# Optimization experiments

Hardware: AMD Instinct MI355X
Metric: run time of the kernel (lower is better)

The kernel has to match this reference:

```python
import jax, jax.numpy as jnp
import numpy as np


def setup_inputs() -> dict:
    key = jax.random.key(0)
    ks = jax.random.split(key, 5)
    bs, ntok, dm, nh = 4, 256, 64, 4
    x = jax.random.normal(ks[0], (bs, ntok, dm), dtype=jnp.float32)
    wk = jax.random.uniform(ks[1], (nh, dm), dtype=jnp.float32)
    wqv_w = jax.random.normal(ks[2], (3 * nh * dm, dm), dtype=jnp.float32) * 0.02
    wqv_b = jnp.zeros((3 * nh * dm,), dtype=jnp.float32)
    fanin_w = jax.random.normal(ks[3], (dm, dm), dtype=jnp.float32) * 0.02
    fanin_b = jnp.zeros((dm,), dtype=jnp.float32)
    return {"x": x, "wk": wk, "wqv_w": wqv_w, "wqv_b": wqv_b,
            "fanin_w": fanin_w, "fanin_b": fanin_b,
            "layer": 0, "use_dp": 0, "doplot": 0}


def reference(x, wk, wqv_w, wqv_b, fanin_w, fanin_b, layer, use_dp, doplot):
    # L1-attention path (use_dp=False, doplot=False) of ResidualAttentionBlock.forward
    bs, ntok, dm = x.shape
    nh = wk.shape[0]
    delta = 0.2
    # wqv projection -> q, vf, vb each [b, t, nh, dm] (d_head == d_model in this module)
    v = (x @ wqv_w.T + wqv_b).reshape(bs, ntok, 3 * nh, dm)
    q, vf, vb = v[:, :, :nh, :], v[:, :, nh:2 * nh, :], v[:, :, 2 * nh:, :]
    k = x[:, :, None, :] * wk[None, None, :, :]   # [b, s, h, w]
    q = q * wk[None, None, :, :]                   # [b, d, h, w]
    # L1Attn: score[b, s, d, h] = -sum_w |q[b,d,h,w] - k[b,s,h,w]| / sqrt(w);
    # module then negates -> positive scaled L1 distance, applies Huber-like remap, negates back.
    dist = jnp.sum(jnp.abs(q[:, None, :, :, :] - k[:, :, None, :, :]), axis=-1)
    dist = dist / jnp.sqrt(jnp.asarray(dm, dtype=x.dtype))  # [b, s, d, h]
    hub = jnp.where(dist < delta, 0.5 * dist * dist, delta * (dist - 0.5 * delta))
    a = -hub
    af = jax.nn.softmax(a, axis=1)                 # softmax over src tokens
    # (ab = softmax over dst and bb are computed in the original but unused: b = bf)
    bf = jnp.einsum('bsdh,bshw->bdhw', af, vf)     # aggregate values over src
    b = jnp.sum(bf, axis=2)                        # sum over heads -> [b, t, dm]
    y = b * jax.nn.sigmoid(1.702 * b)              # QuickGELU
    y = y @ fanin_w.T + fanin_b
    return x + y
```

## Files before the change

### kernel.cpp

```cpp
#include <hip/hip_runtime.h>

#define NT 256
#define DM 64
#define NH 4

__global__ __launch_bounds__(256) void k_proj(const float* __restrict__ x,
                                              const float* __restrict__ wk,
                                              const float* __restrict__ wqv_w,
                                              const float* __restrict__ wqv_b,
                                              float* __restrict__ q_s,
                                              float* __restrict__ vf)
{
    __shared__ float xs[4 * DM];
    const int tid  = threadIdx.x;
    const int tok0 = blockIdx.x * 4;

    if (tid < 64)
        reinterpret_cast<float4*>(xs)[tid] =
            reinterpret_cast<const float4*>(x + tok0 * DM)[tid];
    __syncthreads();

    const float4* wr0 = reinterpret_cast<const float4*>(wqv_w + tid * DM);
    const float4* wr1 = reinterpret_cast<const float4*>(wqv_w + (tid + 256) * DM);
    float a0[4] = {0.f, 0.f, 0.f, 0.f};
    float a1[4] = {0.f, 0.f, 0.f, 0.f};

#pragma unroll
    for (int c4 = 0; c4 < 16; ++c4) {
        const float4 wa = wr0[c4];
        const float4 wb = wr1[c4];
#pragma unroll
        for (int t = 0; t < 4; ++t) {
            const float4 xv = reinterpret_cast<const float4*>(xs + t * DM)[c4];
            a0[t] += xv.x * wa.x + xv.y * wa.y + xv.z * wa.z + xv.w * wa.w;
            a1[t] += xv.x * wb.x + xv.y * wb.y + xv.z * wb.z + xv.w * wb.w;
        }
    }

    const int h = tid >> 6, w = tid & 63;
    const float ba = wqv_b[tid];
    const float bb = wqv_b[tid + 256];
    const float kw = wk[h * DM + w];
#pragma unroll
    for (int t = 0; t < 4; ++t) {
        const int g = tok0 + t, b = g >> 8, tt = g & 255;
        const int o = ((b * NH + h) * NT + tt) * DM + w;
        q_s[o] = (a0[t] + ba) * kw;
        vf[o]  =  a1[t] + bb;
    }
}

#define KS_LD 66
#define AF_LD 258

__global__ __launch_bounds__(256) void k_attn(const float* __restrict__ x,
                                              const float* __restrict__ wk,
                                              const float* __restrict__ q_s,
                                              const float* __restrict__ vf,
                                              float* __restrict__ bf)
{
    __shared__ float ks[64 * KS_LD];
    __shared__ float af[16 * AF_LD];
    __shared__ float vfs[NT * DM];
    __shared__ float part[4 * 16 * DM];

    const int tid = threadIdx.x;
    const int qt  = blockIdx.x;
    const int bh  = blockIdx.y;
    const int b   = bh >> 2, h = bh & 3;
    const int qg  = tid >> 5;
    const int kg  = tid & 31;

    float q0[DM], q1[DM];
    {
        const float4* p0 = reinterpret_cast<const float4*>(
            q_s + ((b * NH + h) * NT + qt * 16 + qg * 2) * DM);
        const float4* p1 = p0 + 16;
#pragma unroll
        for (int i = 0; i < 16; ++i) {
            const float4 u = p0[i];
            q0[4*i] = u.x; q0[4*i+1] = u.y; q0[4*i+2] = u.z; q0[4*i+3] = u.w;
            const float4 v = p1[i];
            q1[4*i] = v.x; q1[4*i+1] = v.y; q1[4*i+2] = v.z; q1[4*i+3] = v.w;
        }
    }

    const float4* wkr = reinterpret_cast<const float4*>(wk + h * DM);

    float dacc[2][8];
#pragma unroll
    for (int j = 0; j < 8; ++j) { dacc[0][j] = 0.f; dacc[1][j] = 0.f; }

    for (int cc = 0; cc < 4; ++cc) {
        __syncthreads();
        {
            const int row = tid >> 2, c0 = (tid & 3) * 16;
            const float4* xp = reinterpret_cast<const float4*>(
                x + ((b * NT) + cc * 64 + row) * DM + c0);
            float* kp = ks + row * KS_LD + c0;
#pragma unroll
            for (int i = 0; i < 4; ++i) {
                const float4 v  = xp[i];
                const float4 wv = wkr[(c0 >> 2) + i];
                reinterpret_cast<float2*>(kp)[2*i]     = make_float2(v.x * wv.x, v.y * wv.y);
                reinterpret_cast<float2*>(kp)[2*i + 1] = make_float2(v.z * wv.z, v.w * wv.w);
            }
        }
        __syncthreads();
#pragma unroll
        for (int k2 = 0; k2 < 2; ++k2) {
            const float2* kp = reinterpret_cast<const float2*>(ks + (kg + 32 * k2) * KS_LD);
            float d0 = 0.f, d1 = 0.f;
#pragma unroll
            for (int c2 = 0; c2 < 32; ++c2) {
                const float2 kv = kp[c2];
                d0 += fabsf(q0[2*c2] - kv.x) + fabsf(q0[2*c2+1] - kv.y);
                d1 += fabsf(q1[2*c2] - kv.x) + fabsf(q1[2*c2+1] - kv.y);
            }
            dacc[0][cc * 2 + k2] = d0;
            dacc[1][cc * 2 + k2] = d1;
        }
    }

    {
        const float4* vp = reinterpret_cast<const float4*>(vf + (b * NH + h) * NT * DM);
#pragma unroll
        for (int it = 0; it < 16; ++it) {
            const int qidx = it * 256 + tid;
            reinterpret_cast<float4*>(vfs)[qidx] = vp[qidx];
        }
    }

    const float delta = 0.2f;
    float aa0[8], aa1[8];
    float m0 = -1e30f, m1 = -1e30f;
#pragma unroll
    for (int j = 0; j < 8; ++j) {
        float d  = dacc[0][j] * 0.125f;
        float hb = (d < delta) ? 0.5f * d * d : delta * (d - 0.5f * delta);
        aa0[j] = -hb; m0 = fmaxf(m0, aa0[j]);
        d  = dacc[1][j] * 0.125f;
        hb = (d < delta) ? 0.5f * d * d : delta * (d - 0.5f * delta);
        aa1[j] = -hb; m1 = fmaxf(m1, aa1[j]);
    }
#pragma unroll
    for (int mask = 1; mask < 32; mask <<= 1) {
        m0 = fmaxf(m0, __shfl_xor(m0, mask, 32));
        m1 = fmaxf(m1, __shfl_xor(m1, mask, 32));
    }
    float s0 = 0.f, s1 = 0.f;
#pragma unroll
    for (int j = 0; j < 8; ++j) {
        aa0[j] = __expf(aa0[j] - m0); s0 += aa0[j];
        aa1[j] = __expf(aa1[j] - m1); s1 += aa1[j];
    }
#pragma unroll
    for (int mask = 1; mask < 32; mask <<= 1) {
        s0 += __shfl_xor(s0, mask, 32);
        s1 += __shfl_xor(s1, mask, 32);
    }
    const float rs0 = 1.f / s0, rs1 = 1.f / s1;
#pragma unroll
    for (int j = 0; j < 8; ++j) {
        const int skey = (j >> 1) * 64 + (j & 1) * 32 + kg;
        af[(qg * 2 + 0) * AF_LD + skey] = aa0[j] * rs0;
        af[(qg * 2 + 1) * AF_LD + skey] = aa1[j] * rs1;
    }
    __syncthreads();

    {
        const int wq  = tid & 15;
        const int qg4 = (tid >> 4) & 3;
        const int sr  = tid >> 6;

        float4 acc0 = {0,0,0,0}, acc1 = {0,0,0,0}, acc2 = {0,0,0,0}, acc3 = {0,0,0,0};
        const float* afb = af + (qg4 * 4) * AF_LD + sr * 64;
        const float* vb  = vfs + (sr * 64) * DM + wq * 4;
#pragma unroll
        for (int s = 0; s < 64; ++s) {
            const float4 v = *reinterpret_cast<const float4*>(vb + s * DM);
            const float a0 = afb[0 * AF_LD + s];
            const float a1 = afb[1 * AF_LD + s];
            const float a2 = afb[2 * AF_LD + s];
            const float a3 = afb[3 * AF_LD + s];
            acc0.x += a0 * v.x; acc0.y += a0 * v.y; acc0.z += a0 * v.z; acc0.w += a0 * v.w;
            acc1.x += a1 * v.x; acc1.y += a1 * v.y; acc1.z += a1 * v.z; acc1.w += a1 * v.w;
            acc2.x += a2 * v.x; acc2.y += a2 * v.y; acc2.z += a2 * v.z; acc2.w += a2 * v.w;
            acc3.x += a3 * v.x; acc3.y += a3 * v.y; acc3.z += a3 * v.z; acc3.w += a3 * v.w;
        }
        float* pp = part + (sr * 16 + qg4 * 4) * DM + wq * 4;
        *reinterpret_cast<float4*>(pp + 0 * DM) = acc0;
        *reinterpret_cast<float4*>(pp + 1 * DM) = acc1;
        *reinterpret_cast<float4*>(pp + 2 * DM) = acc2;
        *reinterpret_cast<float4*>(pp + 3 * DM) = acc3;
    }
    __syncthreads();

    {
        const int q = tid >> 4, w4 = tid & 15;
        const float* pp = part + q * DM + w4 * 4;
        float4 r0 = *reinterpret_cast<const float4*>(pp);
        const float4 r1 = *reinterpret_cast<const float4*>(pp + 16 * DM);
        const float4 r2 = *reinterpret_cast<const float4*>(pp + 32 * DM);
        const float4 r3 = *reinterpret_cast<const float4*>(pp + 48 * DM);
        r0.x += r1.x + r2.x + r3.x;
        r0.y += r1.y + r2.y + r3.y;
        r0.z += r1.z + r2.z + r3.z;
        r0.w += r1.w + r2.w + r3.w;
        float* op = bf + ((b * NH + h) * NT + qt * 16 + q) * DM + w4 * 4;
        *reinterpret_cast<float4*>(op) = r0;
    }
}

__global__ __launch_bounds__(256) void k_out(const float* __restrict__ x,
                                             const float* __restrict__ bf,
                                             const float* __restrict__ fanin_w,
                                             const float* __restrict__ fanin_b,
                                             float* __restrict__ out)
{
    __shared__ float fw[64 * 68];
    __shared__ float ys[4 * DM];

    const int tid  = threadIdx.x;
    const int tok0 = blockIdx.x * 4;

#pragma unroll
    for (int it = 0; it < 4; ++it) {
        const int qidx = it * 256 + tid;
        const int row = qidx >> 4, cq = qidx & 15;
        *reinterpret_cast<float4*>(fw + row * 68 + cq * 4) =
            reinterpret_cast<const float4*>(fanin_w)[qidx];
    }
    {
        const int t = tid >> 6, c = tid & 63;
        const int g = tok0 + t, b = g >> 8, tt = g & 255;
        float s = 0.f;
#pragma unroll
        for (int hh = 0; hh < NH; ++hh)
            s += bf[((b * NH + hh) * NT + tt) * DM + c];
        ys[t * DM + c] = s / (1.f + __expf(-1.702f * s));
    }
    __syncthreads();
    {
        const int t = tid >> 6, w = tid & 63;
        float acc = fanin_b[w];
        const float* yr = ys + t * DM;
        const float* fr = fw + w * 68;
#pragma unroll
        for (int c4 = 0; c4 < 16; ++c4) {
            const float4 yv = *reinterpret_cast<const float4*>(yr + c4 * 4);
            const float4 fv = *reinterpret_cast<const float4*>(fr + c4 * 4);
            acc += yv.x * fv.x + yv.y * fv.y + yv.z * fv.z + yv.w * fv.w;
        }
        const int g = tok0 + t;
        out[g * DM + w] = x[g * DM + w] + acc;
    }
}

extern "C" void kernel_launch(void* const* d_in, const int* in_sizes, int n_in,
                              void* d_out, int out_size, void* d_ws, size_t ws_size,
                              hipStream_t stream) {
    const float* x       = (const float*)d_in[0];
    const float* wk      = (const float*)d_in[1];
    const float* wqv_w   = (const float*)d_in[2];
    const float* wqv_b   = (const float*)d_in[3];
    const float* fanin_w = (const float*)d_in[4];
    const float* fanin_b = (const float*)d_in[5];
    float* out = (float*)d_out;

    float* ws  = (float*)d_ws;
    float* q_s = ws;
    float* vfw = ws + 262144;
    float* bfw = ws + 524288;

    hipLaunchKernelGGL(k_proj, dim3(256),     dim3(256), 0, stream,
                       x, wk, wqv_w, wqv_b, q_s, vfw);
    hipLaunchKernelGGL(k_attn, dim3(16, 16),  dim3(256), 0, stream,
                       x, wk, q_s, vfw, bfw);
    hipLaunchKernelGGL(k_out,  dim3(256),     dim3(256), 0, stream,
                       x, bfw, fanin_w, fanin_b, out);
}
```

Baseline: 100.8 us.

## Widen attention blocks to 1024 threads with one query per wavefront

The attention kernel now runs 1024 threads per block, and each 64-lane wavefront owns one query row instead of each thread handling two queries. Key tiles are double-buffered so the next chunk is staged while the current one is scored. The V tile load moves to the start of the kernel so it overlaps the distance computation. The softmax reduction uses full 64-wide shuffles, and the AV product gives each thread one query and one float4 of output. This cuts per-thread register pressure and the work each thread serializes, in exchange for larger blocks and lower per-thread reuse of each key load.

```diff
diff --git a/kernel.cpp b/kernel.cpp
--- a/kernel.cpp
+++ b/kernel.cpp
@@ -53,162 +53,118 @@
 #define KS_LD 66
 #define AF_LD 258
 
-__global__ __launch_bounds__(256) void k_attn(const float* __restrict__ x,
-                                              const float* __restrict__ wk,
-                                              const float* __restrict__ q_s,
-                                              const float* __restrict__ vf,
-                                              float* __restrict__ bf)
+__global__ __launch_bounds__(1024) void k_attn(const float* __restrict__ x,
+                                               const float* __restrict__ wk,
+                                               const float* __restrict__ q_s,
+                                               const float* __restrict__ vf,
+                                               float* __restrict__ bf)
 {
-    __shared__ float ks[64 * KS_LD];
+    __shared__ float ks[2][64 * KS_LD];
     __shared__ float af[16 * AF_LD];
     __shared__ float vfs[NT * DM];
     __shared__ float part[4 * 16 * DM];
 
-    const int tid = threadIdx.x;
-    const int qt  = blockIdx.x;
-    const int bh  = blockIdx.y;
-    const int b   = bh >> 2, h = bh & 3;
-    const int qg  = tid >> 5;
-    const int kg  = tid & 31;
-
-    float q0[DM], q1[DM];
-    {
-        const float4* p0 = reinterpret_cast<const float4*>(
-            q_s + ((b * NH + h) * NT + qt * 16 + qg * 2) * DM);
-        const float4* p1 = p0 + 16;
+    const int tid  = threadIdx.x;
+    const int qt   = blockIdx.x;
+    const int bh   = blockIdx.y;
+    const int b    = bh >> 2, h = bh & 3;
+    const int wv   = tid >> 6;
+    const int lane = tid & 63;
+
+    {
+        const float4* vp = reinterpret_cast<const float4*>(vf + (size_t)(b * NH + h) * NT * DM);
+        float4* vs = reinterpret_cast<float4*>(vfs);
+#pragma unroll
+        for (int it = 0; it < 4; ++it)
+            vs[it * 1024 + tid] = vp[it * 1024 + tid];
+    }
+
+    float q[DM];
+    {
+        const float4* qp = reinterpret_cast<const float4*>(
+            q_s + (size_t)((b * NH + h) * NT + qt * 16 + wv) * DM);
 #pragma unroll
         for (int i = 0; i < 16; ++i) {
-            const float4 u = p0[i];
-            q0[4*i] = u.x; q0[4*i+1] = u.y; q0[4*i+2] = u.z; q0[4*i+3] = u.w;
-            const float4 v = p1[i];
-            q1[4*i] = v.x; q1[4*i+1] = v.y; q1[4*i+2] = v.z; q1[4*i+3] = v.w;
-        }
-    }
-
-    const float4* wkr = reinterpret_cast<const float4*>(wk + h * DM);
-
-    float dacc[2][8];
-#pragma unroll
-    for (int j = 0; j < 8; ++j) { dacc[0][j] = 0.f; dacc[1][j] = 0.f; }
-
+            const float4 u = qp[i];
+            q[4*i+0] = u.x; q[4*i+1] = u.y; q[4*i+2] = u.z; q[4*i+3] = u.w;
+        }
+    }
+
+    const int srow = tid >> 4;
+    const int sc0  = (tid & 15) * 4;
+    const float4 wv4 = reinterpret_cast<const float4*>(wk + h * DM)[sc0 >> 2];
+    const float* xbase = x + (size_t)b * NT * DM;
+
+    auto STAGE = [&](int cc) {
+        const float4 xv = *reinterpret_cast<const float4*>(
+            xbase + (cc * 64 + srow) * DM + sc0);
+        float* kp = &ks[cc & 1][srow * KS_LD + sc0];
+        reinterpret_cast<float2*>(kp)[0] = make_float2(xv.x * wv4.x, xv.y * wv4.y);
+        reinterpret_cast<float2*>(kp)[1] = make_float2(xv.z * wv4.z, xv.w * wv4.w);
+    };
+
+    float dacc[4];
+    STAGE(0);
+    __syncthreads();
+#pragma unroll
     for (int cc = 0; cc < 4; ++cc) {
+        if (cc < 3) STAGE(cc + 1);
+        const float2* kp = reinterpret_cast<const float2*>(&ks[cc & 1][lane * KS_LD]);
+        float d = 0.f;
+#pragma unroll
+        for (int c2 = 0; c2 < 32; ++c2) {
+            const float2 kv = kp[c2];
+            d += fabsf(q[2*c2] - kv.x) + fabsf(q[2*c2+1] - kv.y);
+        }
+        dacc[cc] = d;
         __syncthreads();
-        {
-            const int row = tid >> 2, c0 = (tid & 3) * 16;
-            const float4* xp = reinterpret_cast<const float4*>(
-                x + ((b * NT) + cc * 64 + row) * DM + c0);
-            float* kp = ks + row * KS_LD + c0;
-#pragma unroll
-            for (int i = 0; i < 4; ++i) {
-                const float4 v  = xp[i];
-                const float4 wv = wkr[(c0 >> 2) + i];
-                reinterpret_cast<float2*>(kp)[2*i]     = make_float2(v.x * wv.x, v.y * wv.y);
-                reinterpret_cast<float2*>(kp)[2*i + 1] = make_float2(v.z * wv.z, v.w * wv.w);
-            }
-        }
-        __syncthreads();
-#pragma unroll
-        for (int k2 = 0; k2 < 2; ++k2) {
-            const float2* kp = reinterpret_cast<const float2*>(ks + (kg + 32 * k2) * KS_LD);
-            float d0 = 0.f, d1 = 0.f;
-#pragma unroll
-            for (int c2 = 0; c2 < 32; ++c2) {
-                const float2 kv = kp[c2];
-                d0 += fabsf(q0[2*c2] - kv.x) + fabsf(q0[2*c2+1] - kv.y);
-                d1 += fabsf(q1[2*c2] - kv.x) + fabsf(q1[2*c2+1] - kv.y);
-            }
-            dacc[0][cc * 2 + k2] = d0;
-            dacc[1][cc * 2 + k2] = d1;
-        }
-    }
-
-    {
-        const float4* vp = reinterpret_cast<const float4*>(vf + (b * NH + h) * NT * DM);
-#pragma unroll
-        for (int it = 0; it < 16; ++it) {
-            const int qidx = it * 256 + tid;
-            reinterpret_cast<float4*>(vfs)[qidx] = vp[qidx];
-        }
     }
 
     const float delta = 0.2f;
-    float aa0[8], aa1[8];
-    float m0 = -1e30f, m1 = -1e30f;
-#pragma unroll
-    for (int j = 0; j < 8; ++j) {
-        float d  = dacc[0][j] * 0.125f;
-        float hb = (d < delta) ? 0.5f * d * d : delta * (d - 0.5f * delta);
-        aa0[j] = -hb; m0 = fmaxf(m0, aa0[j]);
-        d  = dacc[1][j] * 0.125f;
-        hb = (d < delta) ? 0.5f * d * d : delta * (d - 0.5f * delta);
-        aa1[j] = -hb; m1 = fmaxf(m1, aa1[j]);
-    }
-#pragma unroll
-    for (int mask = 1; mask < 32; mask <<= 1) {
-        m0 = fmaxf(m0, __shfl_xor(m0, mask, 32));
-        m1 = fmaxf(m1, __shfl_xor(m1, mask, 32));
-    }
-    float s0 = 0.f, s1 = 0.f;
-#pragma unroll
-    for (int j = 0; j < 8; ++j) {
-        aa0[j] = __expf(aa0[j] - m0); s0 += aa0[j];
-        aa1[j] = __expf(aa1[j] - m1); s1 += aa1[j];
-    }
-#pragma unroll
-    for (int mask = 1; mask < 32; mask <<= 1) {
-        s0 += __shfl_xor(s0, mask, 32);
-        s1 += __shfl_xor(s1, mask, 32);
-    }
-    const float rs0 = 1.f / s0, rs1 = 1.f / s1;
-#pragma unroll
-    for (int j = 0; j < 8; ++j) {
-        const int skey = (j >> 1) * 64 + (j & 1) * 32 + kg;
-        af[(qg * 2 + 0) * AF_LD + skey] = aa0[j] * rs0;
-        af[(qg * 2 + 1) * AF_LD + skey] = aa1[j] * rs1;
-    }
-    __syncthreads();
-
-    {
-        const int wq  = tid & 15;
-        const int qg4 = (tid >> 4) & 3;
-        const int sr  = tid >> 6;
-
-        float4 acc0 = {0,0,0,0}, acc1 = {0,0,0,0}, acc2 = {0,0,0,0}, acc3 = {0,0,0,0};
-        const float* afb = af + (qg4 * 4) * AF_LD + sr * 64;
+    float aa[4], m = -1e30f;
+#pragma unroll
+    for (int j = 0; j < 4; ++j) {
+        const float d  = dacc[j] * 0.125f;
+        const float hb = (d < delta) ? 0.5f * d * d : delta * (d - 0.5f * delta);
+        aa[j] = -hb;
+        m = fmaxf(m, aa[j]);
+    }
+#pragma unroll
+    for (int mask = 1; mask < 64; mask <<= 1)
+        m = fmaxf(m, __shfl_xor(m, mask, 64));
+    float s = 0.f;
+#pragma unroll
+    for (int j = 0; j < 4; ++j) { aa[j] = __expf(aa[j] - m); s += aa[j]; }
+#pragma unroll
+    for (int mask = 1; mask < 64; mask <<= 1)
+        s += __shfl_xor(s, mask, 64);
+    const float rs = 1.f / s;
+#pragma unroll
+    for (int j = 0; j < 4; ++j)
+        af[wv * AF_LD + j * 64 + lane] = aa[j] * rs;
+    __syncthreads();
+
+    {
+        const int wq = tid & 15;
+        const int qq = (tid >> 4) & 15;
+        const int sr = tid >> 8;
+        float4 acc = make_float4(0.f, 0.f, 0.f, 0.f);
+        const float* afr = af + qq * AF_LD + sr * 64;
         const float* vb  = vfs + (sr * 64) * DM + wq * 4;
-#pragma unroll
-        for (int s = 0; s < 64; ++s) {
-            const float4 v = *reinterpret_cast<const float4*>(vb + s * DM);
-            const float a0 = afb[0 * AF_LD + s];
-            const float a1 = afb[1 * AF_LD + s];
-            const float a2 = afb[2 * AF_LD + s];
-            const float a3 = afb[3 * AF_LD + s];
-            acc0.x += a0 * v.x; acc0.y += a0 * v.y; acc0.z += a0 * v.z; acc0.w += a0 * v.w;
-            acc1.x += a1 * v.x; acc1.y += a1 * v.y; acc1.z += a1 * v.z; acc1.w += a1 * v.w;
-            acc2.x += a2 * v.x; acc2.y += a2 * v.y; acc2.z += a2 * v.z; acc2.w += a2 * v.w;
-            acc3.x += a3 * v.x; acc3.y += a3 * v.y; acc3.z += a3 * v.z; acc3.w += a3 * v.w;
-        }
-        float* pp = part + (sr * 16 + qg4 * 4) * DM + wq * 4;
-        *reinterpret_cast<float4*>(pp + 0 * DM) = acc0;
-        *reinterpret_cast<float4*>(pp + 1 * DM) = acc1;
-        *reinterpret_cast<float4*>(pp + 2 * DM) = acc2;
-        *reinterpret_cast<float4*>(pp + 3 * DM) = acc3;
-    }
-    __syncthreads();
-
-    {
-        const int q = tid >> 4, w4 = tid & 15;
-        const float* pp = part + q * DM + w4 * 4;
-        float4 r0 = *reinterpret_cast<const float4*>(pp);
-        const float4 r1 = *reinterpret_cast<const float4*>(pp + 16 * DM);
-        const float4 r2 = *reinterpret_cast<const float4*>(pp + 32 * DM);
-        const float4 r3 = *reinterpret_cast<const float4*>(pp + 48 * DM);
-        r0.x += r1.x + r2.x + r3.x;
-        r0.y += r1.y + r2.y + r3.y;
-        r0.z += r1.z + r2.z + r3.z;
-        r0.w += r1.w + r2.w + r3.w;
-        float* op = bf + ((b * NH + h) * NT + qt * 16 + q) * DM + w4 * 4;
-        *reinterpret_cast<float4*>(op) = r0;
+#pragma unroll 8
+        for (int s2 = 0; s2 < 64; ++s2) {
+            const float a  = afr[s2];
+            const float4 v = *reinterpret_cast<const float4*>(vb + s2 * DM);
+            acc.x += a * v.x; acc.y += a * v.y; acc.z += a * v.z; acc.w += a * v.w;
+        }
+        *reinterpret_cast<float4*>(&part[(sr * 16 + qq) * DM + wq * 4]) = acc;
+    }
+    __syncthreads();
+
+    {
+        const float* pp = part + wv * DM + lane;
+        const float r = pp[0] + pp[1024] + pp[2048] + pp[3072];
+        bf[(size_t)((b * NH + h) * NT + qt * 16 + wv) * DM + lane] = r;
     }
 }
 
@@ -273,10 +229,10 @@
     float* vfw = ws + 262144;
     float* bfw = ws + 524288;
 
-    hipLaunchKernelGGL(k_proj, dim3(256),     dim3(256), 0, stream,
+    hipLaunchKernelGGL(k_proj, dim3(256),    dim3(256),  0, stream,
                        x, wk, wqv_w, wqv_b, q_s, vfw);
-    hipLaunchKernelGGL(k_attn, dim3(16, 16),  dim3(256), 0, stream,
+    hipLaunchKernelGGL(k_attn, dim3(16, 16), dim3(1024), 0, stream,
                        x, wk, q_s, vfw, bfw);
-    hipLaunchKernelGGL(k_out,  dim3(256),     dim3(256), 0, stream,
+    hipLaunchKernelGGL(k_out,  dim3(256),    dim3(256),  0, stream,
                        x, bfw, fanin_w, fanin_b, out);
 }
```

New measurement: 120.6 us. 1.2x slower.
